# Optimization experiments

Measured on AMD Instinct MI355X. Metric: run time of the kernel, lower is better.

Reference implementation:

```python
import jax, jax.numpy as jnp
import numpy as np

BLOCK_SIZE = 32
STRIDE = 16
DIM = 128


def setup_inputs() -> dict:
    key = jax.random.key(0)
    ks = jax.random.split(key, 6)
    B, N, C = 8, 16384, DIM
    x = jax.random.normal(ks[0], (B, N, C), dtype=jnp.float32)
    pos = jax.random.normal(ks[1], (1, BLOCK_SIZE, C), dtype=jnp.float32) * 0.02
    # torch Linear stores W:(out,in); we store transposed (in,out) for x @ W
    fan_in1 = C * BLOCK_SIZE
    W1 = jax.random.uniform(ks[2], (fan_in1, 2 * C), dtype=jnp.float32,
                            minval=-1.0, maxval=1.0) / jnp.sqrt(fan_in1)
    b1 = jax.random.uniform(ks[3], (2 * C,), dtype=jnp.float32,
                            minval=-1.0, maxval=1.0) / jnp.sqrt(fan_in1)
    fan_in2 = 2 * C
    W2 = jax.random.uniform(ks[4], (fan_in2, C), dtype=jnp.float32,
                            minval=-1.0, maxval=1.0) / jnp.sqrt(fan_in2)
    b2 = jax.random.uniform(ks[5], (C,), dtype=jnp.float32,
                            minval=-1.0, maxval=1.0) / jnp.sqrt(fan_in2)
    return {"x": x, "pos": pos, "W1": W1, "b1": b1, "W2": W2, "b2": b2}


def reference(x, pos, W1, b1, W2, b2):
    B, N, C = x.shape
    l, d = BLOCK_SIZE, STRIDE
    if N < l:  # static shapes -> plain Python branch is fine
        return jnp.mean(x, axis=1, keepdims=True)
    num_blocks = (N - l) // d + 1
    # overlapping sliding-window gather: (nb, l) token indices
    idx = jnp.arange(num_blocks)[:, None] * d + jnp.arange(l)[None, :]
    blocks = x[:, idx, :] + pos[None]            # (B, nb, l, C)
    blocks = blocks.reshape(B, num_blocks, l * C)  # (B, nb, l*C)
    h = jax.nn.gelu(blocks @ W1 + b1, approximate=False)  # exact erf GELU (torch default)
    return h @ W2 + b2                           # (B, nb, C)
```

## Files before the change

kernel.cpp:

```cpp
#include <hip/hip_runtime.h>
#include <hip/hip_bf16.h>
#include <math.h>


typedef __attribute__((ext_vector_type(8))) short short8;
typedef __attribute__((ext_vector_type(4))) float f4;

#define OFF_BT   0u
#define OFF_W2T  (2u << 20)
#define OFF_PART ((2u << 20) + (64u << 10))
#define OFF_BIAS ((2u << 20) + (128u << 10))
#define OFF_P    (4u << 20)

static __device__ __forceinline__ unsigned short f2bf(float f) {
  union { float f; unsigned u; } v; v.f = f;
  return (unsigned short)((v.u + 0x7FFFu + ((v.u >> 16) & 1u)) >> 16);
}
static __device__ __forceinline__ float bf2f(unsigned short h) {
  union { unsigned u; float f; } v; v.u = ((unsigned)h) << 16;
  return v.f;
}
static __device__ __forceinline__ void gload_lds16(const void* g, void* l) {
  __builtin_amdgcn_global_load_lds(
      (const __attribute__((address_space(1))) void*)g,
      (__attribute__((address_space(3))) void*)l, 16, 0, 0);
}

__global__ __launch_bounds__(256) void k_prep(const float* __restrict__ W1,
                                              const float* __restrict__ pos,
                                              const float* __restrict__ W2,
                                              unsigned short* __restrict__ Bt,
                                              unsigned short* __restrict__ W2t,
                                              float* __restrict__ part) {
  __shared__ float T[64][65];
  const int w = blockIdx.x;
  const int t = threadIdx.x;
  if (w >= 256) {
    const int n = w - 256;
    W2t[n * 256 + t] = f2bf(W2[t * 128 + n]);
    return;
  }
  const int h = w >> 7, rem = w & 127, kt = rem >> 2, nt = rem & 3;
  const int krow0 = h * 2048 + kt * 64, col0 = nt * 64;
  const int lr = t >> 2, lc = (t & 3) * 16;
  const float* src = W1 + (size_t)(krow0 + lr) * 256 + col0 + lc;
#pragma unroll
  for (int i = 0; i < 4; ++i) {
    f4 v = *(const f4*)(src + i * 4);
#pragma unroll
    for (int q = 0; q < 4; ++q) T[lr][lc + i * 4 + q] = v[q];
  }
  __syncthreads();
  if (t < 64) {
    float s = 0.f;
#pragma unroll 8
    for (int k = 0; k < 64; ++k) s += T[k][t] * pos[krow0 + k];
    part[(h * 32 + kt) * 256 + col0 + t] = s;
  }
  const int nl = t >> 2, kc = (t & 3) * 16;
  short8 o0, o1;
#pragma unroll
  for (int i = 0; i < 8; ++i) o0[i] = (short)f2bf(T[kc + i][nl]);
#pragma unroll
  for (int i = 0; i < 8; ++i) o1[i] = (short)f2bf(T[kc + 8 + i][nl]);
  unsigned short* dst = Bt + (size_t)(256 * h + col0 + nl) * 2048 + kt * 64 + kc;
  *(short8*)dst = o0;
  *(short8*)(dst + 8) = o1;
}

__global__ __launch_bounds__(256) void k_bias(const float* __restrict__ b1,
                                              const float* __restrict__ part,
                                              float* __restrict__ bias) {
  int n = threadIdx.x;
  float s = b1[n];
#pragma unroll 8
  for (int g = 0; g < 64; ++g) s += part[g * 256 + n];
  bias[n] = s;
}

__global__ __launch_bounds__(512, 2) void k_gemm(const float* __restrict__ X,
                                                 const unsigned short* __restrict__ Bt,
                                                 unsigned short* __restrict__ P) {
  __shared__ __align__(16) char lds[2][49152];
  const int orig = blockIdx.x;
  const int wgid = (orig & 7) * 32 + (orig >> 3);
  const int mt = wgid >> 2, nt = wgid & 3;
  const int m0 = mt * 128, n0 = nt * 128;
  const int t = threadIdx.x;
  const int wid = t >> 6, lane = t & 63;
  const int wr = wid >> 1, wc = wid & 1;

  f4 acc[2][4];
#pragma unroll
  for (int m = 0; m < 2; ++m)
#pragma unroll
    for (int n = 0; n < 4; ++n) acc[m][n] = f4{0.f, 0.f, 0.f, 0.f};

#define ISSUE(BUF, KT)                                                     \
  do {                                                                     \
    const int kf = (KT) * 64;                                              \
    _Pragma("unroll") for (int ii = 0; ii < 4; ++ii) {                     \
      const int s = ii * 512 + t;                                          \
      const int row = s >> 4, c16 = s & 15;                                \
      const int e = ((row & 7) << 1) | ((row >> 3) & 1);                   \
      gload_lds16(X + (size_t)(m0 + row) * 2048 + kf + ((c16 ^ e) << 2),   \
                  &lds[BUF][ii * 8192 + wid * 1024]);                      \
    }                                                                      \
    _Pragma("unroll") for (int ii = 0; ii < 2; ++ii) {                     \
      const int s = ii * 512 + t;                                          \
      const int row = s >> 3, c8 = s & 7;                                  \
      gload_lds16(Bt + (size_t)(n0 + row) * 2048 + kf +                    \
                      ((c8 ^ (row & 7)) << 3),                             \
                  &lds[BUF][32768 + ii * 8192 + wid * 1024]);              \
    }                                                                      \
  } while (0)

#define COMPUTE(BUF)                                                       \
  do {                                                                     \
    const float* Ab = (const float*)&lds[BUF][0];                          \
    const unsigned short* Bb = (const unsigned short*)&lds[BUF][32768];    \
    _Pragma("unroll") for (int ks = 0; ks < 2; ++ks) {                     \
      short8 af[2];                                                        \
      short8 bfv[4];                                                       \
      _Pragma("unroll") for (int m = 0; m < 2; ++m) {                      \
        const int row = wr * 32 + m * 16 + (lane & 15);                    \
        const int e = ((row & 7) << 1) | ((row >> 3) & 1);                 \
        const int cp = ks * 8 + (lane >> 4) * 2;                           \
        f4 lo = *(const f4*)(Ab + row * 64 + ((cp ^ e) << 2));             \
        f4 hi = *(const f4*)(Ab + row * 64 + (((cp + 1) ^ e) << 2));       \
        union { short8 s8; unsigned u[4]; } pk;                            \
        asm("v_cvt_pk_bf16_f32 %0, %1, %2" : "=v"(pk.u[0])                 \
            : "v"(lo[0]), "v"(lo[1]));                                     \
        asm("v_cvt_pk_bf16_f32 %0, %1, %2" : "=v"(pk.u[1])                 \
            : "v"(lo[2]), "v"(lo[3]));                                     \
        asm("v_cvt_pk_bf16_f32 %0, %1, %2" : "=v"(pk.u[2])                 \
            : "v"(hi[0]), "v"(hi[1]));                                     \
        asm("v_cvt_pk_bf16_f32 %0, %1, %2" : "=v"(pk.u[3])                 \
            : "v"(hi[2]), "v"(hi[3]));                                     \
        af[m] = pk.s8;                                                     \
      }                                                                    \
      _Pragma("unroll") for (int n = 0; n < 4; ++n) {                      \
        const int row = wc * 64 + n * 16 + (lane & 15);                    \
        const int ch = ks * 4 + (lane >> 4);                               \
        bfv[n] = *(const short8*)(Bb + row * 64 +                          \
                                  ((ch ^ (row & 7)) << 3));                \
      }                                                                    \
      __builtin_amdgcn_s_setprio(1);                                       \
      _Pragma("unroll") for (int m = 0; m < 2; ++m)                        \
        _Pragma("unroll") for (int n = 0; n < 4; ++n)                      \
          acc[m][n] = __builtin_amdgcn_mfma_f32_16x16x32_bf16(             \
              af[m], bfv[n], acc[m][n], 0, 0, 0);                          \
      __builtin_amdgcn_s_setprio(0);                                       \
    }                                                                      \
  } while (0)

  ISSUE(0, 0);
  ISSUE(1, 1);
  __builtin_amdgcn_sched_barrier(0);
  asm volatile("s_waitcnt vmcnt(6)" ::: "memory");
  __builtin_amdgcn_s_barrier();
  __builtin_amdgcn_sched_barrier(0);

#pragma unroll 2
  for (int kt = 0; kt < 32; ++kt) {
    COMPUTE(kt & 1);
    __builtin_amdgcn_sched_barrier(0);
    __builtin_amdgcn_s_barrier();
    __builtin_amdgcn_sched_barrier(0);
    if (kt < 30) {
      ISSUE(kt & 1, kt + 2);
      __builtin_amdgcn_sched_barrier(0);
      asm volatile("s_waitcnt vmcnt(6)" ::: "memory");
      __builtin_amdgcn_s_barrier();
      __builtin_amdgcn_sched_barrier(0);
    } else if (kt == 30) {
      asm volatile("s_waitcnt vmcnt(0)" ::: "memory");
      __builtin_amdgcn_s_barrier();
      __builtin_amdgcn_sched_barrier(0);
    }
  }
#undef ISSUE
#undef COMPUTE

  const int mb = m0 + wr * 32, nb = n0 + wc * 64;
#pragma unroll
  for (int m = 0; m < 2; ++m)
#pragma unroll
    for (int n = 0; n < 4; ++n) {
      const int row0 = mb + m * 16 + ((lane >> 4) << 2);
      const int col = nb + n * 16 + (lane & 15);
#pragma unroll
      for (int r = 0; r < 4; ++r)
        P[(size_t)(row0 + r) * 512 + col] = f2bf(acc[m][n][r]);
    }
}

__global__ __launch_bounds__(256) void k_comb(const unsigned short* __restrict__ P,
                                              const unsigned short* __restrict__ W2t,
                                              const float* __restrict__ bias,
                                              const float* __restrict__ b2,
                                              float* __restrict__ out) {
  __shared__ unsigned short W2s[128 * 256];
  __shared__ unsigned short Hs[32 * 256];
  const int wg = blockIdx.x;
  const int b = wg >> 5, jt = wg & 31;
  const int j0 = jt * 32;
  const int t = threadIdx.x;

  {
    const int row = t >> 1, halfc = (t & 1) * 128;
    const unsigned short* src = W2t + row * 256 + halfc;
    const int cbw = halfc >> 3;
#pragma unroll
    for (int i = 0; i < 16; ++i) {
      short8 v = *(const short8*)(src + i * 8);
      const int c = (cbw + i) ^ (row & 7);
      *(short8*)&W2s[row * 256 + c * 8] = v;
    }
  }
  {
    const int r = t >> 3, seg = t & 7;
    const int j = j0 + r;
    const size_t m = (size_t)b * 1024 + j;
    const size_t mp1 = (j < 1023) ? m + 1 : m;
    const unsigned short* p0 = P + m * 512 + seg * 32;
    const unsigned short* p1 = P + mp1 * 512 + 256 + seg * 32;
    const float* bs = bias + seg * 32;
    const int cbh = seg * 4;
#pragma unroll
    for (int i = 0; i < 4; ++i) {
      short8 v0 = *(const short8*)(p0 + i * 8);
      short8 v1 = *(const short8*)(p1 + i * 8);
      short8 pk;
#pragma unroll
      for (int q = 0; q < 8; ++q) {
        float f = bf2f((unsigned short)v0[q]) + bf2f((unsigned short)v1[q]) +
                  bs[i * 8 + q];
        float g = 0.5f * f * (1.f + erff(f * 0.70710678118f));
        pk[q] = (short)f2bf(g);
      }
      const int c = (cbh + i) ^ (r & 7);
      *(short8*)&Hs[r * 256 + c * 8] = pk;
    }
  }
  __syncthreads();

  const int wid = t >> 6, lane = t & 63;
  f4 acc[2][2];
#pragma unroll
  for (int i = 0; i < 2; ++i)
#pragma unroll
    for (int j = 0; j < 2; ++j) acc[i][j] = f4{0.f, 0.f, 0.f, 0.f};

#pragma unroll
  for (int ks = 0; ks < 8; ++ks) {
    short8 af[2], bfr[2];
    const int cc = ks * 4 + (lane >> 4);
#pragma unroll
    for (int f = 0; f < 2; ++f) {
      const int ra = f * 16 + (lane & 15);
      af[f] = *(const short8*)&Hs[ra * 256 + ((cc ^ (ra & 7)) << 3)];
      const int rb = wid * 32 + f * 16 + (lane & 15);
      bfr[f] = *(const short8*)&W2s[rb * 256 + ((cc ^ (rb & 7)) << 3)];
    }
#pragma unroll
    for (int i = 0; i < 2; ++i)
#pragma unroll
      for (int j = 0; j < 2; ++j)
        acc[i][j] = __builtin_amdgcn_mfma_f32_16x16x32_bf16(af[i], bfr[j],
                                                            acc[i][j], 0, 0, 0);
  }
#pragma unroll
  for (int i = 0; i < 2; ++i)
#pragma unroll
    for (int j = 0; j < 2; ++j) {
      const int row0 = i * 16 + ((lane >> 4) << 2);
      const int col = wid * 32 + j * 16 + (lane & 15);
      const float bb = b2[col];
#pragma unroll
      for (int r = 0; r < 4; ++r) {
        const int jj = j0 + row0 + r;
        if (jj < 1023)
          out[((size_t)b * 1023 + jj) * 128 + col] = acc[i][j][r] + bb;
      }
    }
}

extern "C" void kernel_launch(void* const* d_in, const int* in_sizes, int n_in,
                              void* d_out, int out_size, void* d_ws, size_t ws_size,
                              hipStream_t stream) {
  const float* x   = (const float*)d_in[0];
  const float* pos = (const float*)d_in[1];
  const float* W1  = (const float*)d_in[2];
  const float* b1  = (const float*)d_in[3];
  const float* W2  = (const float*)d_in[4];
  const float* b2  = (const float*)d_in[5];
  float* out = (float*)d_out;
  char* ws = (char*)d_ws;
  unsigned short* Bt  = (unsigned short*)(ws + OFF_BT);
  unsigned short* W2t = (unsigned short*)(ws + OFF_W2T);
  float* part         = (float*)(ws + OFF_PART);
  float* bias         = (float*)(ws + OFF_BIAS);
  unsigned short* P   = (unsigned short*)(ws + OFF_P);

  k_prep<<<384, 256, 0, stream>>>(W1, pos, W2, Bt, W2t, part);
  k_bias<<<1, 256, 0, stream>>>(b1, part, bias);
  k_gemm<<<256, 512, 0, stream>>>(x, Bt, P);
  k_comb<<<256, 256, 0, stream>>>(P, W2t, bias, b2, out);
}
```

Measured before the change: 53.91 us.

## Split GEMM K dimension in two and sum partials in combine kernel

The main GEMM now splits the K=2048 reduction into two halves, launching 512 workgroups of 256 threads, each with a 64x64 per-wave tile and 32-wide K steps. Each half writes its own bf16 partial buffer, and the combine kernel reads both halves and sums them before the GELU. This raises the workgroup count to fill more CUs and cuts LDS per block, at the cost of twice the partial-output traffic and an extra bf16 rounding of each partial.

```diff
diff --git a/kernel.cpp b/kernel.cpp
--- a/kernel.cpp
+++ b/kernel.cpp
@@ -78,80 +78,78 @@
   bias[n] = s;
 }
 
-__global__ __launch_bounds__(512, 2) void k_gemm(const float* __restrict__ X,
+__global__ __launch_bounds__(256, 2) void k_gemm(const float* __restrict__ X,
                                                  const unsigned short* __restrict__ Bt,
                                                  unsigned short* __restrict__ P) {
-  __shared__ __align__(16) char lds[2][49152];
+  __shared__ __align__(16) char lds[2][24576];
   const int orig = blockIdx.x;
-  const int wgid = (orig & 7) * 32 + (orig >> 3);
-  const int mt = wgid >> 2, nt = wgid & 3;
-  const int m0 = mt * 128, n0 = nt * 128;
+  const int wg = (orig & 7) * 64 + (orig >> 3);
+  const int mt = wg >> 3;
+  const int nt = (wg >> 1) & 3;
+  const int ksp = wg & 1;
+  const int m0 = mt * 128, n0 = nt * 128, k0 = ksp * 1024;
   const int t = threadIdx.x;
   const int wid = t >> 6, lane = t & 63;
-  const int wr = wid >> 1, wc = wid & 1;
-
-  f4 acc[2][4];
-#pragma unroll
-  for (int m = 0; m < 2; ++m)
-#pragma unroll
-    for (int n = 0; n < 4; ++n) acc[m][n] = f4{0.f, 0.f, 0.f, 0.f};
+  const int wm = (wid >> 1) * 64, wn = (wid & 1) * 64;
+
+  f4 acc[4][4];
+#pragma unroll
+  for (int i = 0; i < 4; ++i)
+#pragma unroll
+    for (int j = 0; j < 4; ++j) acc[i][j] = f4{0.f, 0.f, 0.f, 0.f};
 
 #define ISSUE(BUF, KT)                                                     \
   do {                                                                     \
-    const int kf = (KT) * 64;                                              \
+    const int kf = k0 + (KT) * 32;                                         \
     _Pragma("unroll") for (int ii = 0; ii < 4; ++ii) {                     \
-      const int s = ii * 512 + t;                                          \
-      const int row = s >> 4, c16 = s & 15;                                \
-      const int e = ((row & 7) << 1) | ((row >> 3) & 1);                   \
-      gload_lds16(X + (size_t)(m0 + row) * 2048 + kf + ((c16 ^ e) << 2),   \
-                  &lds[BUF][ii * 8192 + wid * 1024]);                      \
+      const int s = ii * 256 + t;                                          \
+      const int row = s >> 3, c8 = s & 7;                                  \
+      gload_lds16(X + (size_t)(m0 + row) * 2048 + kf +                     \
+                      ((c8 ^ (row & 7)) << 2),                             \
+                  &lds[BUF][ii * 4096 + wid * 1024]);                      \
     }                                                                      \
     _Pragma("unroll") for (int ii = 0; ii < 2; ++ii) {                     \
-      const int s = ii * 512 + t;                                          \
-      const int row = s >> 3, c8 = s & 7;                                  \
+      const int s = ii * 256 + t;                                          \
+      const int row = s >> 2, c4 = s & 3;                                  \
       gload_lds16(Bt + (size_t)(n0 + row) * 2048 + kf +                    \
-                      ((c8 ^ (row & 7)) << 3),                             \
-                  &lds[BUF][32768 + ii * 8192 + wid * 1024]);              \
+                      ((c4 ^ (row & 3)) << 3),                             \
+                  &lds[BUF][16384 + ii * 4096 + wid * 1024]);              \
     }                                                                      \
   } while (0)
 
 #define COMPUTE(BUF)                                                       \
   do {                                                                     \
     const float* Ab = (const float*)&lds[BUF][0];                          \
-    const unsigned short* Bb = (const unsigned short*)&lds[BUF][32768];    \
-    _Pragma("unroll") for (int ks = 0; ks < 2; ++ks) {                     \
-      short8 af[2];                                                        \
-      short8 bfv[4];                                                       \
-      _Pragma("unroll") for (int m = 0; m < 2; ++m) {                      \
-        const int row = wr * 32 + m * 16 + (lane & 15);                    \
-        const int e = ((row & 7) << 1) | ((row >> 3) & 1);                 \
-        const int cp = ks * 8 + (lane >> 4) * 2;                           \
-        f4 lo = *(const f4*)(Ab + row * 64 + ((cp ^ e) << 2));             \
-        f4 hi = *(const f4*)(Ab + row * 64 + (((cp + 1) ^ e) << 2));       \
-        union { short8 s8; unsigned u[4]; } pk;                            \
-        asm("v_cvt_pk_bf16_f32 %0, %1, %2" : "=v"(pk.u[0])                 \
-            : "v"(lo[0]), "v"(lo[1]));                                     \
-        asm("v_cvt_pk_bf16_f32 %0, %1, %2" : "=v"(pk.u[1])                 \
-            : "v"(lo[2]), "v"(lo[3]));                                     \
-        asm("v_cvt_pk_bf16_f32 %0, %1, %2" : "=v"(pk.u[2])                 \
-            : "v"(hi[0]), "v"(hi[1]));                                     \
-        asm("v_cvt_pk_bf16_f32 %0, %1, %2" : "=v"(pk.u[3])                 \
-            : "v"(hi[2]), "v"(hi[3]));                                     \
-        af[m] = pk.s8;                                                     \
-      }                                                                    \
-      _Pragma("unroll") for (int n = 0; n < 4; ++n) {                      \
-        const int row = wc * 64 + n * 16 + (lane & 15);                    \
-        const int ch = ks * 4 + (lane >> 4);                               \
-        bfv[n] = *(const short8*)(Bb + row * 64 +                          \
-                                  ((ch ^ (row & 7)) << 3));                \
-      }                                                                    \
-      __builtin_amdgcn_s_setprio(1);                                       \
-      _Pragma("unroll") for (int m = 0; m < 2; ++m)                        \
-        _Pragma("unroll") for (int n = 0; n < 4; ++n)                      \
-          acc[m][n] = __builtin_amdgcn_mfma_f32_16x16x32_bf16(             \
-              af[m], bfv[n], acc[m][n], 0, 0, 0);                          \
-      __builtin_amdgcn_s_setprio(0);                                       \
+    const unsigned short* Bb = (const unsigned short*)&lds[BUF][16384];    \
+    short8 af[4], bfv[4];                                                  \
+    const int jk = lane >> 4;                                              \
+    _Pragma("unroll") for (int m = 0; m < 4; ++m) {                        \
+      const int row = wm + m * 16 + (lane & 15);                           \
+      const int e = row & 7;                                               \
+      f4 lo = *(const f4*)(Ab + row * 32 + (((2 * jk) ^ e) << 2));         \
+      f4 hi = *(const f4*)(Ab + row * 32 + (((2 * jk + 1) ^ e) << 2));     \
+      union { short8 s8; unsigned u[4]; } pk;                              \
+      asm("v_cvt_pk_bf16_f32 %0, %1, %2" : "=v"(pk.u[0])                   \
+          : "v"(lo[0]), "v"(lo[1]));                                       \
+      asm("v_cvt_pk_bf16_f32 %0, %1, %2" : "=v"(pk.u[1])                   \
+          : "v"(lo[2]), "v"(lo[3]));                                       \
+      asm("v_cvt_pk_bf16_f32 %0, %1, %2" : "=v"(pk.u[2])                   \
+          : "v"(hi[0]), "v"(hi[1]));                                       \
+      asm("v_cvt_pk_bf16_f32 %0, %1, %2" : "=v"(pk.u[3])                   \
+          : "v"(hi[2]), "v"(hi[3]));                                       \
+      af[m] = pk.s8;                                                       \
     }                                                                      \
+    _Pragma("unroll") for (int n = 0; n < 4; ++n) {                        \
+      const int row = wn + n * 16 + (lane & 15);                           \
+      bfv[n] = *(const short8*)(Bb + row * 32 +                            \
+                                ((jk ^ (row & 3)) << 3));                  \
+    }                                                                      \
+    __builtin_amdgcn_s_setprio(1);                                         \
+    _Pragma("unroll") for (int m = 0; m < 4; ++m)                          \
+      _Pragma("unroll") for (int n = 0; n < 4; ++n)                        \
+        acc[m][n] = __builtin_amdgcn_mfma_f32_16x16x32_bf16(               \
+            af[m], bfv[n], acc[m][n], 0, 0, 0);                            \
+    __builtin_amdgcn_s_setprio(0);                                         \
   } while (0)
 
   ISSUE(0, 0);
@@ -182,16 +180,17 @@
 #undef ISSUE
 #undef COMPUTE
 
-  const int mb = m0 + wr * 32, nb = n0 + wc * 64;
-#pragma unroll
-  for (int m = 0; m < 2; ++m)
+  unsigned short* Pp = P + (size_t)ksp * (8192 * 512);
+  const int mb = m0 + wm, nb = n0 + wn;
+#pragma unroll
+  for (int m = 0; m < 4; ++m)
 #pragma unroll
     for (int n = 0; n < 4; ++n) {
       const int row0 = mb + m * 16 + ((lane >> 4) << 2);
       const int col = nb + n * 16 + (lane & 15);
 #pragma unroll
       for (int r = 0; r < 4; ++r)
-        P[(size_t)(row0 + r) * 512 + col] = f2bf(acc[m][n][r]);
+        Pp[(size_t)(row0 + r) * 512 + col] = f2bf(acc[m][n][r]);
     }
 }
 
@@ -202,6 +201,8 @@
                                               float* __restrict__ out) {
   __shared__ unsigned short W2s[128 * 256];
   __shared__ unsigned short Hs[32 * 256];
+  const unsigned short* Pa = P;
+  const unsigned short* Pb = P + (size_t)8192 * 512;
   const int wg = blockIdx.x;
   const int b = wg >> 5, jt = wg & 31;
   const int j0 = jt * 32;
@@ -223,18 +224,23 @@
     const int j = j0 + r;
     const size_t m = (size_t)b * 1024 + j;
     const size_t mp1 = (j < 1023) ? m + 1 : m;
-    const unsigned short* p0 = P + m * 512 + seg * 32;
-    const unsigned short* p1 = P + mp1 * 512 + 256 + seg * 32;
+    const unsigned short* p0a = Pa + m * 512 + seg * 32;
+    const unsigned short* p0b = Pb + m * 512 + seg * 32;
+    const unsigned short* p1a = Pa + mp1 * 512 + 256 + seg * 32;
+    const unsigned short* p1b = Pb + mp1 * 512 + 256 + seg * 32;
     const float* bs = bias + seg * 32;
     const int cbh = seg * 4;
 #pragma unroll
     for (int i = 0; i < 4; ++i) {
-      short8 v0 = *(const short8*)(p0 + i * 8);
-      short8 v1 = *(const short8*)(p1 + i * 8);
+      short8 v0a = *(const short8*)(p0a + i * 8);
+      short8 v0b = *(const short8*)(p0b + i * 8);
+      short8 v1a = *(const short8*)(p1a + i * 8);
+      short8 v1b = *(const short8*)(p1b + i * 8);
       short8 pk;
 #pragma unroll
       for (int q = 0; q < 8; ++q) {
-        float f = bf2f((unsigned short)v0[q]) + bf2f((unsigned short)v1[q]) +
+        float f = bf2f((unsigned short)v0a[q]) + bf2f((unsigned short)v0b[q]) +
+                  bf2f((unsigned short)v1a[q]) + bf2f((unsigned short)v1b[q]) +
                   bs[i * 8 + q];
         float g = 0.5f * f * (1.f + erff(f * 0.70710678118f));
         pk[q] = (short)f2bf(g);
@@ -305,6 +311,6 @@
 
   k_prep<<<384, 256, 0, stream>>>(W1, pos, W2, Bt, W2t, part);
   k_bias<<<1, 256, 0, stream>>>(b1, part, bias);
-  k_gemm<<<256, 512, 0, stream>>>(x, Bt, P);
+  k_gemm<<<512, 256, 0, stream>>>(x, Bt, P);
   k_comb<<<256, 256, 0, stream>>>(P, W2t, bias, b2, out);
 }
```

Result: no change. 54.14 us (+0.4%).

## Load A fragments directly from global to registers, stage only B in LDS

Applied to the files above, without the earlier changes.

The GEMM kernel stops staging the fp32 activation tile in LDS. Each wave now loads its own A fragments straight from global memory into registers, double-buffered in registers across k-substeps, while only the bf16 weight tile goes through LDS with larger 128-wide k chunks and fewer barriers. This removes LDS capacity and bandwidth pressure plus LDS round trips for A, and the launch-bounds occupancy hint is dropped. The cost is uncoalesced or duplicated global reads of A, since the two column-waves read the same rows, and higher register use.

```diff
diff --git a/kernel.cpp b/kernel.cpp
--- a/kernel.cpp
+++ b/kernel.cpp
@@ -78,17 +78,19 @@
   bias[n] = s;
 }
 
-__global__ __launch_bounds__(512, 2) void k_gemm(const float* __restrict__ X,
-                                                 const unsigned short* __restrict__ Bt,
-                                                 unsigned short* __restrict__ P) {
-  __shared__ __align__(16) char lds[2][49152];
+__global__ __launch_bounds__(512) void k_gemm(const float* __restrict__ X,
+                                              const unsigned short* __restrict__ Bt,
+                                              unsigned short* __restrict__ P) {
+  __shared__ __align__(16) unsigned short Bl[2][128 * 128];
   const int orig = blockIdx.x;
-  const int wgid = (orig & 7) * 32 + (orig >> 3);
-  const int mt = wgid >> 2, nt = wgid & 3;
+  const int wg = (orig & 7) * 32 + (orig >> 3);
+  const int mt = wg >> 2, nt = wg & 3;
   const int m0 = mt * 128, n0 = nt * 128;
   const int t = threadIdx.x;
   const int wid = t >> 6, lane = t & 63;
   const int wr = wid >> 1, wc = wid & 1;
+  const float* Abase =
+      X + (size_t)(m0 + wr * 32 + (lane & 15)) * 2048 + (lane >> 4) * 8;
 
   f4 acc[2][4];
 #pragma unroll
@@ -96,90 +98,92 @@
 #pragma unroll
     for (int n = 0; n < 4; ++n) acc[m][n] = f4{0.f, 0.f, 0.f, 0.f};
 
-#define ISSUE(BUF, KT)                                                     \
+  f4 a0[2][2], a1[2][2];
+
+#define LOADA(DST, KCOL)                                                   \
   do {                                                                     \
-    const int kf = (KT) * 64;                                              \
+    _Pragma("unroll") for (int f = 0; f < 2; ++f) {                        \
+      DST[f][0] = *(const f4*)(Abase + f * 32768 + (KCOL));                \
+      DST[f][1] = *(const f4*)(Abase + f * 32768 + (KCOL) + 4);            \
+    }                                                                      \
+  } while (0)
+
+#define ISSUE_B(BUF, CI)                                                   \
+  do {                                                                     \
     _Pragma("unroll") for (int ii = 0; ii < 4; ++ii) {                     \
       const int s = ii * 512 + t;                                          \
       const int row = s >> 4, c16 = s & 15;                                \
-      const int e = ((row & 7) << 1) | ((row >> 3) & 1);                   \
-      gload_lds16(X + (size_t)(m0 + row) * 2048 + kf + ((c16 ^ e) << 2),   \
-                  &lds[BUF][ii * 8192 + wid * 1024]);                      \
-    }                                                                      \
-    _Pragma("unroll") for (int ii = 0; ii < 2; ++ii) {                     \
-      const int s = ii * 512 + t;                                          \
-      const int row = s >> 3, c8 = s & 7;                                  \
-      gload_lds16(Bt + (size_t)(n0 + row) * 2048 + kf +                    \
-                      ((c8 ^ (row & 7)) << 3),                             \
-                  &lds[BUF][32768 + ii * 8192 + wid * 1024]);              \
+      gload_lds16(Bt + (size_t)(n0 + row) * 2048 + (CI) * 128 +            \
+                      ((c16 ^ (row & 15)) << 3),                           \
+                  (char*)&Bl[BUF][0] + ii * 8192 + wid * 1024);            \
     }                                                                      \
   } while (0)
 
-#define COMPUTE(BUF)                                                       \
+#define COMPUTE(BUF, S, ASRC)                                              \
   do {                                                                     \
-    const float* Ab = (const float*)&lds[BUF][0];                          \
-    const unsigned short* Bb = (const unsigned short*)&lds[BUF][32768];    \
-    _Pragma("unroll") for (int ks = 0; ks < 2; ++ks) {                     \
-      short8 af[2];                                                        \
-      short8 bfv[4];                                                       \
-      _Pragma("unroll") for (int m = 0; m < 2; ++m) {                      \
-        const int row = wr * 32 + m * 16 + (lane & 15);                    \
-        const int e = ((row & 7) << 1) | ((row >> 3) & 1);                 \
-        const int cp = ks * 8 + (lane >> 4) * 2;                           \
-        f4 lo = *(const f4*)(Ab + row * 64 + ((cp ^ e) << 2));             \
-        f4 hi = *(const f4*)(Ab + row * 64 + (((cp + 1) ^ e) << 2));       \
-        union { short8 s8; unsigned u[4]; } pk;                            \
-        asm("v_cvt_pk_bf16_f32 %0, %1, %2" : "=v"(pk.u[0])                 \
-            : "v"(lo[0]), "v"(lo[1]));                                     \
-        asm("v_cvt_pk_bf16_f32 %0, %1, %2" : "=v"(pk.u[1])                 \
-            : "v"(lo[2]), "v"(lo[3]));                                     \
-        asm("v_cvt_pk_bf16_f32 %0, %1, %2" : "=v"(pk.u[2])                 \
-            : "v"(hi[0]), "v"(hi[1]));                                     \
-        asm("v_cvt_pk_bf16_f32 %0, %1, %2" : "=v"(pk.u[3])                 \
-            : "v"(hi[2]), "v"(hi[3]));                                     \
-        af[m] = pk.s8;                                                     \
-      }                                                                    \
-      _Pragma("unroll") for (int n = 0; n < 4; ++n) {                      \
-        const int row = wc * 64 + n * 16 + (lane & 15);                    \
-        const int ch = ks * 4 + (lane >> 4);                               \
-        bfv[n] = *(const short8*)(Bb + row * 64 +                          \
-                                  ((ch ^ (row & 7)) << 3));                \
-      }                                                                    \
-      __builtin_amdgcn_s_setprio(1);                                       \
-      _Pragma("unroll") for (int m = 0; m < 2; ++m)                        \
-        _Pragma("unroll") for (int n = 0; n < 4; ++n)                      \
-          acc[m][n] = __builtin_amdgcn_mfma_f32_16x16x32_bf16(             \
-              af[m], bfv[n], acc[m][n], 0, 0, 0);                          \
-      __builtin_amdgcn_s_setprio(0);                                       \
+    short8 af[2], bf[4];                                                   \
+    _Pragma("unroll") for (int f = 0; f < 2; ++f) {                        \
+      union { short8 s8; unsigned u[4]; } pk;                              \
+      asm("v_cvt_pk_bf16_f32 %0, %1, %2" : "=v"(pk.u[0])                   \
+          : "v"(ASRC[f][0][0]), "v"(ASRC[f][0][1]));                       \
+      asm("v_cvt_pk_bf16_f32 %0, %1, %2" : "=v"(pk.u[1])                   \
+          : "v"(ASRC[f][0][2]), "v"(ASRC[f][0][3]));                       \
+      asm("v_cvt_pk_bf16_f32 %0, %1, %2" : "=v"(pk.u[2])                   \
+          : "v"(ASRC[f][1][0]), "v"(ASRC[f][1][1]));                       \
+      asm("v_cvt_pk_bf16_f32 %0, %1, %2" : "=v"(pk.u[3])                   \
+          : "v"(ASRC[f][1][2]), "v"(ASRC[f][1][3]));                       \
+      af[f] = pk.s8;                                                       \
     }                                                                      \
+    _Pragma("unroll") for (int j = 0; j < 4; ++j) {                        \
+      const int row = wc * 64 + j * 16 + (lane & 15);                      \
+      const int c16 = (S) * 4 + (lane >> 4);                               \
+      bf[j] = *(const short8*)&Bl[BUF][row * 128 +                         \
+                                       ((c16 ^ (row & 15)) << 3)];         \
+    }                                                                      \
+    __builtin_amdgcn_s_setprio(1);                                         \
+    _Pragma("unroll") for (int f = 0; f < 2; ++f)                          \
+      _Pragma("unroll") for (int j = 0; j < 4; ++j)                        \
+        acc[f][j] = __builtin_amdgcn_mfma_f32_16x16x32_bf16(               \
+            af[f], bf[j], acc[f][j], 0, 0, 0);                             \
+    __builtin_amdgcn_s_setprio(0);                                         \
   } while (0)
 
-  ISSUE(0, 0);
-  ISSUE(1, 1);
+  LOADA(a0, 0);
+  ISSUE_B(0, 0);
+  ISSUE_B(1, 1);
   __builtin_amdgcn_sched_barrier(0);
-  asm volatile("s_waitcnt vmcnt(6)" ::: "memory");
+  asm volatile("s_waitcnt vmcnt(4)" ::: "memory");
   __builtin_amdgcn_s_barrier();
   __builtin_amdgcn_sched_barrier(0);
 
-#pragma unroll 2
-  for (int kt = 0; kt < 32; ++kt) {
-    COMPUTE(kt & 1);
+  for (int ci = 0; ci < 16; ++ci) {
+    const int buf = ci & 1;
+    const int ck = ci * 128;
+    LOADA(a1, ck + 32);
+    COMPUTE(buf, 0, a0);
+    LOADA(a0, ck + 64);
+    COMPUTE(buf, 1, a1);
+    LOADA(a1, ck + 96);
+    COMPUTE(buf, 2, a0);
+    if (ci < 15) LOADA(a0, ck + 128);
+    COMPUTE(buf, 3, a1);
+    if (ci == 15) break;
     __builtin_amdgcn_sched_barrier(0);
     __builtin_amdgcn_s_barrier();
     __builtin_amdgcn_sched_barrier(0);
-    if (kt < 30) {
-      ISSUE(kt & 1, kt + 2);
+    if (ci < 14) {
+      ISSUE_B(buf, ci + 2);
       __builtin_amdgcn_sched_barrier(0);
-      asm volatile("s_waitcnt vmcnt(6)" ::: "memory");
-      __builtin_amdgcn_s_barrier();
+      asm volatile("s_waitcnt vmcnt(8)" ::: "memory");
+    } else {
       __builtin_amdgcn_sched_barrier(0);
-    } else if (kt == 30) {
-      asm volatile("s_waitcnt vmcnt(0)" ::: "memory");
-      __builtin_amdgcn_s_barrier();
-      __builtin_amdgcn_sched_barrier(0);
-    }
-  }
-#undef ISSUE
+      asm volatile("s_waitcnt vmcnt(4)" ::: "memory");
+    }
+    __builtin_amdgcn_s_barrier();
+    __builtin_amdgcn_sched_barrier(0);
+  }
+#undef LOADA
+#undef ISSUE_B
 #undef COMPUTE
 
   const int mb = m0 + wr * 32, nb = n0 + wc * 64;
```

New measurement: 96.02 us. 78.1% more time.

## Triple-buffer GEMM LDS pipeline and fold bias reduction into combine kernel

Applied to the files above, without the earlier changes.

The GEMM kernel moves from a double-buffered to a triple-buffered LDS pipeline, prefetching three K-tiles ahead with adjusted vmcnt waits. The launch-bounds occupancy hint of two blocks per CU is dropped, since 144KB of LDS per block allows only one. The separate single-block bias-reduction kernel is removed and each combine block recomputes the bias sum into shared memory. This saves one launch but repeats the 64-way reduction in every combine block, and lower GEMM occupancy may hurt latency hiding.

```diff
diff --git a/kernel.cpp b/kernel.cpp
--- a/kernel.cpp
+++ b/kernel.cpp
@@ -9,7 +9,6 @@
 #define OFF_BT   0u
 #define OFF_W2T  (2u << 20)
 #define OFF_PART ((2u << 20) + (64u << 10))
-#define OFF_BIAS ((2u << 20) + (128u << 10))
 #define OFF_P    (4u << 20)
 
 static __device__ __forceinline__ unsigned short f2bf(float f) {
@@ -68,20 +67,10 @@
   *(short8*)(dst + 8) = o1;
 }
 
-__global__ __launch_bounds__(256) void k_bias(const float* __restrict__ b1,
-                                              const float* __restrict__ part,
-                                              float* __restrict__ bias) {
-  int n = threadIdx.x;
-  float s = b1[n];
-#pragma unroll 8
-  for (int g = 0; g < 64; ++g) s += part[g * 256 + n];
-  bias[n] = s;
-}
-
-__global__ __launch_bounds__(512, 2) void k_gemm(const float* __restrict__ X,
-                                                 const unsigned short* __restrict__ Bt,
-                                                 unsigned short* __restrict__ P) {
-  __shared__ __align__(16) char lds[2][49152];
+__global__ __launch_bounds__(512) void k_gemm(const float* __restrict__ X,
+                                              const unsigned short* __restrict__ Bt,
+                                              unsigned short* __restrict__ P) {
+  __shared__ __align__(16) char lds[3][49152];
   const int orig = blockIdx.x;
   const int wgid = (orig & 7) * 32 + (orig >> 3);
   const int mt = wgid >> 2, nt = wgid & 3;
@@ -156,20 +145,24 @@
 
   ISSUE(0, 0);
   ISSUE(1, 1);
+  ISSUE(2, 2);
   __builtin_amdgcn_sched_barrier(0);
-  asm volatile("s_waitcnt vmcnt(6)" ::: "memory");
+  asm volatile("s_waitcnt vmcnt(12)" ::: "memory");
   __builtin_amdgcn_s_barrier();
   __builtin_amdgcn_sched_barrier(0);
 
-#pragma unroll 2
   for (int kt = 0; kt < 32; ++kt) {
-    COMPUTE(kt & 1);
+    COMPUTE(kt % 3);
     __builtin_amdgcn_sched_barrier(0);
     __builtin_amdgcn_s_barrier();
     __builtin_amdgcn_sched_barrier(0);
-    if (kt < 30) {
-      ISSUE(kt & 1, kt + 2);
+    if (kt < 29) {
+      ISSUE(kt % 3, kt + 3);
       __builtin_amdgcn_sched_barrier(0);
+      asm volatile("s_waitcnt vmcnt(12)" ::: "memory");
+      __builtin_amdgcn_s_barrier();
+      __builtin_amdgcn_sched_barrier(0);
+    } else if (kt == 29) {
       asm volatile("s_waitcnt vmcnt(6)" ::: "memory");
       __builtin_amdgcn_s_barrier();
       __builtin_amdgcn_sched_barrier(0);
@@ -197,17 +190,25 @@
 
 __global__ __launch_bounds__(256) void k_comb(const unsigned short* __restrict__ P,
                                               const unsigned short* __restrict__ W2t,
-                                              const float* __restrict__ bias,
+                                              const float* __restrict__ part,
+                                              const float* __restrict__ b1,
                                               const float* __restrict__ b2,
                                               float* __restrict__ out) {
   __shared__ unsigned short W2s[128 * 256];
   __shared__ unsigned short Hs[32 * 256];
+  __shared__ float biasS[256];
   const int wg = blockIdx.x;
   const int b = wg >> 5, jt = wg & 31;
   const int j0 = jt * 32;
   const int t = threadIdx.x;
 
   {
+    float s = b1[t];
+#pragma unroll 8
+    for (int g = 0; g < 64; ++g) s += part[g * 256 + t];
+    biasS[t] = s;
+  }
+  {
     const int row = t >> 1, halfc = (t & 1) * 128;
     const unsigned short* src = W2t + row * 256 + halfc;
     const int cbw = halfc >> 3;
@@ -218,6 +219,7 @@
       *(short8*)&W2s[row * 256 + c * 8] = v;
     }
   }
+  __syncthreads();
   {
     const int r = t >> 3, seg = t & 7;
     const int j = j0 + r;
@@ -225,7 +227,7 @@
     const size_t mp1 = (j < 1023) ? m + 1 : m;
     const unsigned short* p0 = P + m * 512 + seg * 32;
     const unsigned short* p1 = P + mp1 * 512 + 256 + seg * 32;
-    const float* bs = bias + seg * 32;
+    const float* bs = biasS + seg * 32;
     const int cbh = seg * 4;
 #pragma unroll
     for (int i = 0; i < 4; ++i) {
@@ -300,11 +302,9 @@
   unsigned short* Bt  = (unsigned short*)(ws + OFF_BT);
   unsigned short* W2t = (unsigned short*)(ws + OFF_W2T);
   float* part         = (float*)(ws + OFF_PART);
-  float* bias         = (float*)(ws + OFF_BIAS);
   unsigned short* P   = (unsigned short*)(ws + OFF_P);
 
   k_prep<<<384, 256, 0, stream>>>(W1, pos, W2, Bt, W2t, part);
-  k_bias<<<1, 256, 0, stream>>>(b1, part, bias);
   k_gemm<<<256, 512, 0, stream>>>(x, Bt, P);
-  k_comb<<<256, 256, 0, stream>>>(P, W2t, bias, b2, out);
-}
+  k_comb<<<256, 256, 0, stream>>>(P, W2t, part, b1, b2, out);
+}
```

After: 52.36 us. -2.9%, faster.
